# Optimization experiments

Hardware: AMD Instinct MI355X
Metric: run time of the kernel (lower is better)

## Reference

```python
import jax, jax.numpy as jnp
import numpy as np

DIM = 128
D_STATE = 16
EXPAND = 2
E = DIM * EXPAND
BSZ, H, W = 16, 64, 64
LN_EPS = 1e-5


def setup_inputs() -> dict:
    key = jax.random.key(0)
    ks = jax.random.split(key, 8)
    s_in = 1.0 / np.sqrt(DIM)
    s_out = 1.0 / np.sqrt(E)
    return {
        "x": jax.random.normal(ks[0], (BSZ, DIM, H, W), jnp.float32),
        "A": jax.random.normal(ks[1], (D_STATE, D_STATE), jnp.float32) * 0.1,
        "Bm": jax.random.normal(ks[2], (D_STATE, E), jnp.float32) * 0.1,
        "Cm": jax.random.normal(ks[3], (E, D_STATE), jnp.float32) * 0.1,
        "D": jax.random.normal(ks[4], (E,), jnp.float32) * 0.1,
        "W_in": jax.random.uniform(ks[5], (E, DIM), jnp.float32, -s_in, s_in),
        "b_in": jnp.zeros((E,), jnp.float32),
        "W_out": jax.random.uniform(ks[6], (DIM, E), jnp.float32, -s_out, s_out),
        "b_out": jnp.zeros((DIM,), jnp.float32),
        "gamma": jnp.ones((DIM,), jnp.float32),
        "beta": jnp.zeros((DIM,), jnp.float32),
    }


def reference(x, A, Bm, Cm, D, W_in, b_in, W_out, b_out, gamma, beta):
    # x: [B, C, H, W]; dropout is inference-mode identity
    Bsz, C, Hh, Ww = x.shape
    residual = x
    h = x.transpose(0, 2, 3, 1).reshape(Bsz, Hh * Ww, C)  # [B, L, C]
    # LayerNorm over channel dim
    mu = jnp.mean(h, axis=-1, keepdims=True)
    var = jnp.mean((h - mu) ** 2, axis=-1, keepdims=True)
    hn = (h - mu) * jax.lax.rsqrt(var + LN_EPS) * gamma + beta
    # in_proj
    z = jnp.einsum('blc,ec->ble', hn, W_in) + b_in  # [B, L, E]
    # precompute input drive for the recurrence: x_t @ B.T
    u = jnp.einsum('ble,se->bls', z, Bm)  # [B, L, S]
    u_tm = u.transpose(1, 0, 2)  # [L, B, S] time-major for scan

    def step(state, u_t):
        state = jnp.tanh(state @ A.T + u_t)
        return state, state

    init = jnp.zeros((Bsz, A.shape[0]), z.dtype)
    _, states = jax.lax.scan(step, init, u_tm)  # states: [L, B, S]
    states = states.transpose(1, 0, 2)  # [B, L, S]
    y = jnp.einsum('bls,es->ble', states, Cm) + z * D  # [B, L, E]
    out = jnp.einsum('ble,ce->blc', y, W_out) + b_out  # [B, L, C]
    out = out.reshape(Bsz, Hh, Ww, C).transpose(0, 3, 1, 2)
    return out + residual
```

## Files before the change

kernel.cpp:

```cpp
#include <hip/hip_runtime.h>
#include <cstdint>

#define BATCH 16
#define CDIM  128
#define EDIM  256
#define SDIM  16
#define LSEQ  4096
#define LN_EPS 1e-5f

typedef __attribute__((ext_vector_type(8))) short short8;
typedef __attribute__((ext_vector_type(4))) float f32x4;
typedef __attribute__((ext_vector_type(4))) unsigned int u32x4;

#define BIASC  20480
#define BU     20608
#define WCF    20736
#define WUF    41216
#define U_OFF  65536

static __device__ __forceinline__ unsigned short f2bf(float f) {
    uint32_t u = __float_as_uint(f);
    uint32_t r = u + 0x7fffu + ((u >> 16) & 1u);
    return (unsigned short)(r >> 16);
}
static __device__ __forceinline__ float bf2f(unsigned short h) {
    return __uint_as_float(((uint32_t)h) << 16);
}
static __device__ __forceinline__ uint32_t pack_split_trunc(float v) {
    uint32_t u = __float_as_uint(v);
    float hi_f = __uint_as_float(u & 0xffff0000u);
    unsigned short lo = f2bf(v - hi_f);
    return (u >> 16) | ((uint32_t)lo << 16);
}

union U4S8 { u32x4 u; short8 s; };

static __device__ __forceinline__ uint32_t permb(uint32_t a, uint32_t b, uint32_t sel) {
    return __builtin_amdgcn_perm(a, b, sel);
}

static __device__ __forceinline__ void load_bfrag(const uint32_t* row, int cb, int sw,
                                                  short8& bh, short8& bl) {
    u32x4 A = *reinterpret_cast<const u32x4*>(&row[(cb) ^ sw]);
    u32x4 B = *reinterpret_cast<const u32x4*>(&row[(cb + 4) ^ sw]);
    U4S8 h, l;
    h.u[0] = permb(A[1], A[0], 0x05040100u);
    h.u[1] = permb(A[3], A[2], 0x05040100u);
    h.u[2] = permb(B[1], B[0], 0x05040100u);
    h.u[3] = permb(B[3], B[2], 0x05040100u);
    l.u[0] = permb(A[1], A[0], 0x07060302u);
    l.u[1] = permb(A[3], A[2], 0x07060302u);
    l.u[2] = permb(B[1], B[0], 0x07060302u);
    l.u[3] = permb(B[3], B[2], 0x07060302u);
    bh = h.s; bl = l.s;
}

#define MFMA(acc, a, b) acc = __builtin_amdgcn_mfma_f32_16x16x32_bf16((a), (b), (acc), 0, 0, 0)

#define ROT_I(VAL, K) __builtin_amdgcn_mov_dpp((VAL), 0x120 + (K), 0xF, 0xF, true)
#define REP15(M) M(1) M(2) M(3) M(4) M(5) M(6) M(7) M(8) M(9) M(10) M(11) M(12) M(13) M(14) M(15)

#if __has_builtin(__builtin_amdgcn_rcpf)
  #define RCPF(x) __builtin_amdgcn_rcpf(x)
#else
  #define RCPF(x) (1.0f / (x))
#endif

#define SCAN_STEP(ST, UT) { \
    float a0 = fmaf(Ak[0], (ST), (UT)); \
    float a1 = 0.f, a2 = 0.f, a3 = 0.f; \
    { \
        float r_; \
        r_ = __int_as_float(ROT_I(__float_as_int(ST), 1));  a1 = fmaf(Ak[1],  r_, a1); \
        r_ = __int_as_float(ROT_I(__float_as_int(ST), 2));  a2 = fmaf(Ak[2],  r_, a2); \
        r_ = __int_as_float(ROT_I(__float_as_int(ST), 3));  a3 = fmaf(Ak[3],  r_, a3); \
        r_ = __int_as_float(ROT_I(__float_as_int(ST), 4));  a0 = fmaf(Ak[4],  r_, a0); \
        r_ = __int_as_float(ROT_I(__float_as_int(ST), 5));  a1 = fmaf(Ak[5],  r_, a1); \
        r_ = __int_as_float(ROT_I(__float_as_int(ST), 6));  a2 = fmaf(Ak[6],  r_, a2); \
        r_ = __int_as_float(ROT_I(__float_as_int(ST), 7));  a3 = fmaf(Ak[7],  r_, a3); \
        r_ = __int_as_float(ROT_I(__float_as_int(ST), 8));  a0 = fmaf(Ak[8],  r_, a0); \
        r_ = __int_as_float(ROT_I(__float_as_int(ST), 9));  a1 = fmaf(Ak[9],  r_, a1); \
        r_ = __int_as_float(ROT_I(__float_as_int(ST), 10)); a2 = fmaf(Ak[10], r_, a2); \
        r_ = __int_as_float(ROT_I(__float_as_int(ST), 11)); a3 = fmaf(Ak[11], r_, a3); \
        r_ = __int_as_float(ROT_I(__float_as_int(ST), 12)); a0 = fmaf(Ak[12], r_, a0); \
        r_ = __int_as_float(ROT_I(__float_as_int(ST), 13)); a1 = fmaf(Ak[13], r_, a1); \
        r_ = __int_as_float(ROT_I(__float_as_int(ST), 14)); a2 = fmaf(Ak[14], r_, a2); \
        r_ = __int_as_float(ROT_I(__float_as_int(ST), 15)); a3 = fmaf(Ak[15], r_, a3); \
    } \
    float X = (a0 + a2) + (a1 + a3); \
    float ex = __expf(X + X); \
    (ST) = fmaf(-2.f, RCPF(ex + 1.f), 1.f); }

__global__ __launch_bounds__(256) void prep_kernel(
    const float* __restrict__ Bm, const float* __restrict__ Cm,
    const float* __restrict__ Dv, const float* __restrict__ W_in,
    const float* __restrict__ b_in, const float* __restrict__ W_out,
    const float* __restrict__ b_out, float* __restrict__ ws)
{
    uint32_t* wsu = (uint32_t*)ws;
    int blk = blockIdx.x, tid = threadIdx.x;
    if (blk < 40) {
        int widx = blk * 256 + tid;
        int j2 = widx & 3;
        int l  = (widx >> 2) & 63;
        int mf = (widx >> 8) & 7;
        int kt = widx >> 11;
        int row = mf * 16 + (l & 15);
        int k0 = kt * 32 + ((l >> 4) << 3) + j2 * 2;
        float v0 = 0.f, v1 = 0.f;
        if (kt < 4) {
            #pragma unroll 4
            for (int e = 0; e < EDIM; ++e) {
                float wd = W_out[row * EDIM + e] * Dv[e];
                v0 = fmaf(wd, W_in[e * CDIM + k0], v0);
                v1 = fmaf(wd, W_in[e * CDIM + k0 + 1], v1);
            }
        } else {
            int s0 = k0 - 128;
            if (s0 < 16) {
                #pragma unroll 4
                for (int e = 0; e < EDIM; ++e) {
                    float wo = W_out[row * EDIM + e];
                    v0 = fmaf(wo, Cm[e * SDIM + s0], v0);
                    v1 = fmaf(wo, Cm[e * SDIM + s0 + 1], v1);
                }
            }
        }
        unsigned short h0 = f2bf(v0), h1 = f2bf(v1);
        unsigned short l0 = f2bf(v0 - bf2f(h0));
        unsigned short l1 = f2bf(v1 - bf2f(h1));
        wsu[WCF + widx]         = (uint32_t)h0 | ((uint32_t)h1 << 16);
        wsu[WCF + 10240 + widx] = (uint32_t)l0 | ((uint32_t)l1 << 16);
    } else if (blk < 44) {
        int widx = (blk - 40) * 256 + tid;
        int j2 = widx & 3;
        int l  = (widx >> 2) & 63;
        int kt = (widx >> 8) & 3;
        int row = l & 15;
        int k0 = kt * 32 + ((l >> 4) << 3) + j2 * 2;
        float v0 = 0.f, v1 = 0.f;
        #pragma unroll 4
        for (int e = 0; e < EDIM; ++e) {
            float bm = Bm[row * EDIM + e];
            v0 = fmaf(bm, W_in[e * CDIM + k0], v0);
            v1 = fmaf(bm, W_in[e * CDIM + k0 + 1], v1);
        }
        unsigned short h0 = f2bf(v0), h1 = f2bf(v1);
        unsigned short l0 = f2bf(v0 - bf2f(h0));
        unsigned short l1 = f2bf(v1 - bf2f(h1));
        wsu[WUF + widx]        = (uint32_t)h0 | ((uint32_t)h1 << 16);
        wsu[WUF + 1024 + widx] = (uint32_t)l0 | ((uint32_t)l1 << 16);
    } else {
        if (tid < 128) {
            float acc = b_out[tid];
            #pragma unroll 4
            for (int e = 0; e < EDIM; ++e)
                acc += W_out[tid * EDIM + e] * Dv[e] * b_in[e];
            ws[BIASC + tid] = acc;
        } else if (tid < 144) {
            int s = tid - 128;
            float acc = 0.f;
            #pragma unroll 4
            for (int e = 0; e < EDIM; ++e)
                acc += Bm[s * EDIM + e] * b_in[e];
            ws[BU + s] = acc;
        }
    }
}

__global__ __launch_bounds__(256) void halo_kernel(
    const float* __restrict__ x, const float* __restrict__ gamma,
    const float* __restrict__ beta, float* __restrict__ ws)
{
    __shared__ uint32_t xs2[32 * 128];
    __shared__ float pr1[4][32], pr2[4][32];
    __shared__ float mu2[32], rs2[32];
    __shared__ float ulh[32 * 16];

    int t = threadIdx.x;
    int lane = t & 63, wv = t >> 6;
    int blk = blockIdx.x;
    int b  = blk >> 5;
    int P0 = (blk & 31) << 7;
    const float* xb = x + ((size_t)b * CDIM) * LSEQ + P0 + 96;
    const uint32_t* wsu = (const uint32_t*)ws;

    int q4 = 4 * ((t >> 3) & 7);
    f32x4 xr[4];
    float sm0=0.f,sm1=0.f,sm2=0.f,sm3=0.f, sq0=0.f,sq1=0.f,sq2=0.f,sq3=0.f;
    #pragma unroll
    for (int it = 0; it < 4; ++it) {
        int c = (t & 7) + 32 * wv + 8 * it;
        f32x4 v = *reinterpret_cast<const f32x4*>(xb + (size_t)c * LSEQ + q4);
        xr[it] = v;
        sm0 += v[0]; sq0 += v[0]*v[0];
        sm1 += v[1]; sq1 += v[1]*v[1];
        sm2 += v[2]; sq2 += v[2]*v[2];
        sm3 += v[3]; sq3 += v[3]*v[3];
    }
    sm0 += __shfl_xor(sm0,1); sm0 += __shfl_xor(sm0,2); sm0 += __shfl_xor(sm0,4);
    sm1 += __shfl_xor(sm1,1); sm1 += __shfl_xor(sm1,2); sm1 += __shfl_xor(sm1,4);
    sm2 += __shfl_xor(sm2,1); sm2 += __shfl_xor(sm2,2); sm2 += __shfl_xor(sm2,4);
    sm3 += __shfl_xor(sm3,1); sm3 += __shfl_xor(sm3,2); sm3 += __shfl_xor(sm3,4);
    sq0 += __shfl_xor(sq0,1); sq0 += __shfl_xor(sq0,2); sq0 += __shfl_xor(sq0,4);
    sq1 += __shfl_xor(sq1,1); sq1 += __shfl_xor(sq1,2); sq1 += __shfl_xor(sq1,4);
    sq2 += __shfl_xor(sq2,1); sq2 += __shfl_xor(sq2,2); sq2 += __shfl_xor(sq2,4);
    sq3 += __shfl_xor(sq3,1); sq3 += __shfl_xor(sq3,2); sq3 += __shfl_xor(sq3,4);
    if ((lane & 7) == 0) {
        pr1[wv][q4+0] = sm0; pr2[wv][q4+0] = sq0;
        pr1[wv][q4+1] = sm1; pr2[wv][q4+1] = sq1;
        pr1[wv][q4+2] = sm2; pr2[wv][q4+2] = sq2;
        pr1[wv][q4+3] = sm3; pr2[wv][q4+3] = sq3;
    }
    __syncthreads();
    if (t < 32) {
        float s1 = pr1[0][t] + pr1[1][t] + pr1[2][t] + pr1[3][t];
        float s2 = pr2[0][t] + pr2[1][t] + pr2[2][t] + pr2[3][t];
        float mu = s1 * (1.f / 128.f);
        float var = s2 * (1.f / 128.f) - mu * mu;
        mu2[t] = mu; rs2[t] = rsqrtf(var + LN_EPS);
    }
    __syncthreads();

    {
        float mu_[4], rs_[4];
        #pragma unroll
        for (int j = 0; j < 4; ++j) { mu_[j] = mu2[q4+j]; rs_[j] = rs2[q4+j]; }
        #pragma unroll
        for (int it = 0; it < 4; ++it) {
            int c = (t & 7) + 32 * wv + 8 * it;
            float g = gamma[c], be = beta[c];
            #pragma unroll
            for (int j = 0; j < 4; ++j) {
                int q = q4 + j;
                float val = (xr[it][j] - mu_[j]) * rs_[j] * g + be;
                xs2[q * 128 + (c ^ (((q >> 1) & 7) << 2))] = pack_split_trunc(val);
            }
        }
    }
    __syncthreads();

    if (wv < 2) {
        short8 auh[4], aul[4];
        #pragma unroll
        for (int kt = 0; kt < 4; ++kt) {
            U4S8 tt;
            tt.u = *reinterpret_cast<const u32x4*>(&wsu[WUF + kt * 256 + lane * 4]);
            auh[kt] = tt.s;
            tt.u = *reinterpret_cast<const u32x4*>(&wsu[WUF + 1024 + kt * 256 + lane * 4]);
            aul[kt] = tt.s;
        }
        int q = wv * 16 + (lane & 15);
        const uint32_t* row = xs2 + q * 128;
        int sw = ((q >> 1) & 7) << 2;
        f32x4 acc = {0.f, 0.f, 0.f, 0.f};
        #pragma unroll
        for (int kt = 0; kt < 4; ++kt) {
            short8 bh, bl;
            load_bfrag(row, kt * 32 + ((lane >> 4) << 3), sw, bh, bl);
            MFMA(acc, auh[kt], bh);
            MFMA(acc, auh[kt], bl);
            MFMA(acc, aul[kt], bh);
        }
        int s4 = (lane >> 4) << 2;
        f32x4 bu4 = *reinterpret_cast<const f32x4*>(ws + BU + s4);
        #pragma unroll
        for (int j = 0; j < 4; ++j)
            ulh[q * 16 + s4 + j] = acc[j] + bu4[j];
    }
    __syncthreads();
    if (t < 128)
        *reinterpret_cast<f32x4*>(ws + U_OFF + (size_t)blk * 512 + t * 4) =
            *reinterpret_cast<const f32x4*>(ulh + t * 4);
}

__global__ __launch_bounds__(256, 2) void fused_kernel(
    const float* __restrict__ x, const float* __restrict__ Amat,
    const float* __restrict__ gamma, const float* __restrict__ beta,
    float* __restrict__ out, const float* __restrict__ ws)
{
    __shared__ uint32_t xs[16384];
    __shared__ unsigned short ul[160 * 18];
    __shared__ unsigned short stl[128 * 32];
    __shared__ float mu_s[128], sig_s[128];

    int t = threadIdx.x;
    int lane = t & 63, wv = t >> 6;
    int blk = blockIdx.x;
    int b  = blk >> 5;
    int P0 = (blk & 31) << 7;
    const float* xb = x   + ((size_t)b * CDIM) * LSEQ + P0;
    float*       ob = out + ((size_t)b * CDIM) * LSEQ + P0;
    const uint32_t* wsu = (const uint32_t*)ws;

    int p4 = 4 * (t >> 3);
    {
        f32x4 xr[16];
        float sm0=0.f,sm1=0.f,sm2=0.f,sm3=0.f, sq0=0.f,sq1=0.f,sq2=0.f,sq3=0.f;
        #pragma unroll
        for (int it = 0; it < 16; ++it) {
            int c = (t & 7) + 8 * it;
            f32x4 v = *reinterpret_cast<const f32x4*>(xb + (size_t)c * LSEQ + p4);
            xr[it] = v;
            sm0 += v[0]; sq0 += v[0]*v[0];
            sm1 += v[1]; sq1 += v[1]*v[1];
            sm2 += v[2]; sq2 += v[2]*v[2];
            sm3 += v[3]; sq3 += v[3]*v[3];
        }
        sm0 += __shfl_xor(sm0,1); sm0 += __shfl_xor(sm0,2); sm0 += __shfl_xor(sm0,4);
        sm1 += __shfl_xor(sm1,1); sm1 += __shfl_xor(sm1,2); sm1 += __shfl_xor(sm1,4);
        sm2 += __shfl_xor(sm2,1); sm2 += __shfl_xor(sm2,2); sm2 += __shfl_xor(sm2,4);
        sm3 += __shfl_xor(sm3,1); sm3 += __shfl_xor(sm3,2); sm3 += __shfl_xor(sm3,4);
        sq0 += __shfl_xor(sq0,1); sq0 += __shfl_xor(sq0,2); sq0 += __shfl_xor(sq0,4);
        sq1 += __shfl_xor(sq1,1); sq1 += __shfl_xor(sq1,2); sq1 += __shfl_xor(sq1,4);
        sq2 += __shfl_xor(sq2,1); sq2 += __shfl_xor(sq2,2); sq2 += __shfl_xor(sq2,4);
        sq3 += __shfl_xor(sq3,1); sq3 += __shfl_xor(sq3,2); sq3 += __shfl_xor(sq3,4);
        float mu_[4], rs_[4], sg_[4];
        {
            float smv[4] = {sm0, sm1, sm2, sm3};
            float sqv[4] = {sq0, sq1, sq2, sq3};
            #pragma unroll
            for (int j = 0; j < 4; ++j) {
                float mu = smv[j] * (1.f / 128.f);
                float var = sqv[j] * (1.f / 128.f) - mu * mu;
                float rs = rsqrtf(var + LN_EPS);
                mu_[j] = mu; rs_[j] = rs; sg_[j] = RCPF(rs);
            }
        }
        if ((lane & 7) == 0) {
            #pragma unroll
            for (int j = 0; j < 4; ++j) { mu_s[p4+j] = mu_[j]; sig_s[p4+j] = sg_[j]; }
        }
        #pragma unroll
        for (int it = 0; it < 16; ++it) {
            int c = (t & 7) + 8 * it;
            float g = gamma[c], be = beta[c];
            #pragma unroll
            for (int j = 0; j < 4; ++j) {
                int p = p4 + j;
                float val = (xr[it][j] - mu_[j]) * rs_[j] * g + be;
                xs[p * 128 + (c ^ (((p >> 1) & 7) << 2))] = pack_split_trunc(val);
            }
        }
    }
    __syncthreads();

    {
        if (t < 128) {
            int src = (blk & 31) ? (blk - 1) : (blk > 0 ? blk : 0);
            f32x4 v = *reinterpret_cast<const f32x4*>(ws + U_OFF + (size_t)src * 512 + t * 4);
            int q = t >> 2, s0 = (t & 3) * 4;
            #pragma unroll
            for (int k = 0; k < 4; ++k)
                ul[q * 18 + s0 + k] = f2bf(v[k]);
        }
        {
            uint32_t* stl32 = (uint32_t*)stl;
            int p = t >> 1, k0 = 8 + (t & 1) * 4;
            u32x4 z = {0u,0u,0u,0u};
            *reinterpret_cast<u32x4*>(&stl32[p * 16 + k0]) = z;
        }
        short8 auh[4], aul[4];
        #pragma unroll
        for (int kt = 0; kt < 4; ++kt) {
            U4S8 tt;
            tt.u = *reinterpret_cast<const u32x4*>(&wsu[WUF + kt * 256 + lane * 4]);
            auh[kt] = tt.s;
            tt.u = *reinterpret_cast<const u32x4*>(&wsu[WUF + 1024 + kt * 256 + lane * 4]);
            aul[kt] = tt.s;
        }
        int s4 = (lane >> 4) << 2;
        f32x4 bu4 = *reinterpret_cast<const f32x4*>(ws + BU + s4);
        #pragma unroll
        for (int nfi = 0; nfi < 2; ++nfi) {
            int nf = wv * 2 + nfi;
            int p = nf * 16 + (lane & 15);
            const uint32_t* row = xs + p * 128;
            int sw = ((p >> 1) & 7) << 2;
            f32x4 acc = {0.f, 0.f, 0.f, 0.f};
            #pragma unroll
            for (int kt = 0; kt < 4; ++kt) {
                short8 bh, bl;
                load_bfrag(row, kt * 32 + ((lane >> 4) << 3), sw, bh, bl);
                MFMA(acc, auh[kt], bh);
                MFMA(acc, auh[kt], bl);
                MFMA(acc, aul[kt], bh);
            }
            #pragma unroll
            for (int j = 0; j < 4; ++j)
                ul[(32 + p) * 18 + s4 + j] = f2bf(acc[j] + bu4[j]);
        }
    }
    __syncthreads();

    {
        int s = t & 15, g = t >> 4;
        float Ak[16];
        Ak[0] = Amat[s * 16 + s];
        {
            int pk;
            #define PERMLOAD(K) pk = ROT_I(s, K); Ak[K] = Amat[s * 16 + pk];
            REP15(PERMLOAD)
            #undef PERMLOAD
        }
        int r0 = 8 * g;
        float ub[8];
        #pragma unroll
        for (int j = 0; j < 8; ++j) ub[j] = bf2f(ul[(r0 + j) * 18 + s]);
        int rl = r0 + 8;
        int tbase = P0 + 8 * g - 32;
        float st = 0.f;
        #pragma unroll
        for (int it = 0; it < 4; ++it) {
            #pragma unroll
            for (int j = 0; j < 8; ++j) {
                float u_t = (tbase + it * 8 + j >= 0) ? ub[j] : 0.f;
                ub[j] = bf2f(ul[rl * 18 + s]);
                ++rl;
                SCAN_STEP(st, u_t)
            }
        }
        #pragma unroll
        for (int j = 0; j < 8; ++j) {
            SCAN_STEP(st, ub[j])
            stl[(r0 + j) * 32 + s] = f2bf(st);
        }
    }
    __syncthreads();

    int wm = wv >> 1, wn = wv & 1;
    f32x4 acc[4][4];
    #pragma unroll
    for (int mf = 0; mf < 4; ++mf)
        #pragma unroll
        for (int nfl = 0; nfl < 4; ++nfl) { f32x4 z = {0.f,0.f,0.f,0.f}; acc[mf][nfl] = z; }

    #pragma unroll 2
    for (int kt = 0; kt < 4; ++kt) {
        short8 ah[4], al[4];
        #pragma unroll
        for (int mf = 0; mf < 4; ++mf) {
            int mfg = wm * 4 + mf;
            U4S8 tt;
            tt.u = *reinterpret_cast<const u32x4*>(&wsu[WCF + (kt * 8 + mfg) * 256 + lane * 4]);
            ah[mf] = tt.s;
            tt.u = *reinterpret_cast<const u32x4*>(&wsu[WCF + 10240 + (kt * 8 + mfg) * 256 + lane * 4]);
            al[mf] = tt.s;
        }
        #pragma unroll
        for (int nfl = 0; nfl < 4; ++nfl) {
            int p = (wn * 4 + nfl) * 16 + (lane & 15);
            const uint32_t* row = xs + p * 128;
            short8 bh, bl;
            load_bfrag(row, kt * 32 + ((lane >> 4) << 3), ((p >> 1) & 7) << 2, bh, bl);
            #pragma unroll
            for (int mf = 0; mf < 4; ++mf) {
                MFMA(acc[mf][nfl], ah[mf], bh);
                MFMA(acc[mf][nfl], ah[mf], bl);
                MFMA(acc[mf][nfl], al[mf], bh);
            }
        }
    }
    {
        short8 ah[4];
        #pragma unroll
        for (int mf = 0; mf < 4; ++mf) {
            int mfg = wm * 4 + mf;
            U4S8 tt;
            tt.u = *reinterpret_cast<const u32x4*>(&wsu[WCF + (32 + mfg) * 256 + lane * 4]);
            ah[mf] = tt.s;
        }
        int grp = lane >> 4;
        #pragma unroll
        for (int nfl = 0; nfl < 4; ++nfl) {
            int p = (wn * 4 + nfl) * 16 + (lane & 15);
            U4S8 tt;
            tt.u = *reinterpret_cast<const u32x4*>(&stl[p * 32 + grp * 8]);
            short8 bs = tt.s;
            #pragma unroll
            for (int mf = 0; mf < 4; ++mf)
                MFMA(acc[mf][nfl], ah[mf], bs);
        }
    }

    {
        int q4 = (lane >> 4) << 2;
        float sgp[4], mup[4];
        #pragma unroll
        for (int nfl = 0; nfl < 4; ++nfl) {
            int p = (wn * 4 + nfl) * 16 + (lane & 15);
            sgp[nfl] = sig_s[p]; mup[nfl] = mu_s[p];
        }
        #pragma unroll
        for (int mf = 0; mf < 4; ++mf) {
            int cb = wm * 64 + mf * 16 + q4;
            f32x4 bc = *reinterpret_cast<const f32x4*>(ws + BIASC + cb);
            #pragma unroll
            for (int j = 0; j < 4; ++j) {
                int c = cb + j;
                float ig = RCPF(gamma[c]);
                float be = beta[c];
                size_t rowa = (size_t)c * LSEQ;
                #pragma unroll
                for (int nfl = 0; nfl < 4; ++nfl) {
                    int p = (wn * 4 + nfl) * 16 + (lane & 15);
                    uint32_t w = xs[p * 128 + (c ^ (((p >> 1) & 7) << 2))];
                    float hn = __uint_as_float(w << 16) + __uint_as_float(w & 0xffff0000u);
                    float xrc = fmaf((hn - be) * ig, sgp[nfl], mup[nfl]);
                    float val = acc[mf][nfl][j] + bc[j] + xrc;
                    __builtin_nontemporal_store(val, &ob[rowa + p]);
                }
            }
        }
    }
}

extern "C" void kernel_launch(void* const* d_in, const int* in_sizes, int n_in,
                              void* d_out, int out_size, void* d_ws, size_t ws_size,
                              hipStream_t stream)
{
    const float* x     = (const float*)d_in[0];
    const float* A     = (const float*)d_in[1];
    const float* Bm    = (const float*)d_in[2];
    const float* Cm    = (const float*)d_in[3];
    const float* Dv    = (const float*)d_in[4];
    const float* W_in  = (const float*)d_in[5];
    const float* b_in  = (const float*)d_in[6];
    const float* W_out = (const float*)d_in[7];
    const float* b_out = (const float*)d_in[8];
    const float* gamma = (const float*)d_in[9];
    const float* beta  = (const float*)d_in[10];
    float* ws  = (float*)d_ws;
    float* out = (float*)d_out;

    prep_kernel <<<dim3(45),  dim3(256), 0, stream>>>(Bm, Cm, Dv, W_in, b_in, W_out, b_out, ws);
    halo_kernel <<<dim3(512), dim3(256), 0, stream>>>(x, gamma, beta, ws);
    fused_kernel<<<dim3(512), dim3(256), 0, stream>>>(x, A, gamma, beta, out, ws);
}
```

Measured before the change: 139.6 us.

## Drop split-bf16 GEMMs, fuse halo into main kernel, re-read residual from global

```diff
diff --git a/kernel.cpp b/kernel.cpp
--- a/kernel.cpp
+++ b/kernel.cpp
@@ -16,7 +16,6 @@
 #define BU     20608
 #define WCF    20736
 #define WUF    41216
-#define U_OFF  65536
 
 static __device__ __forceinline__ unsigned short f2bf(float f) {
     uint32_t u = __float_as_uint(f);
@@ -26,34 +25,11 @@
 static __device__ __forceinline__ float bf2f(unsigned short h) {
     return __uint_as_float(((uint32_t)h) << 16);
 }
-static __device__ __forceinline__ uint32_t pack_split_trunc(float v) {
-    uint32_t u = __float_as_uint(v);
-    float hi_f = __uint_as_float(u & 0xffff0000u);
-    unsigned short lo = f2bf(v - hi_f);
-    return (u >> 16) | ((uint32_t)lo << 16);
+static __device__ __forceinline__ uint32_t pack2bf(float a, float b) {
+    return (uint32_t)f2bf(a) | ((uint32_t)f2bf(b) << 16);
 }
 
 union U4S8 { u32x4 u; short8 s; };
-
-static __device__ __forceinline__ uint32_t permb(uint32_t a, uint32_t b, uint32_t sel) {
-    return __builtin_amdgcn_perm(a, b, sel);
-}
-
-static __device__ __forceinline__ void load_bfrag(const uint32_t* row, int cb, int sw,
-                                                  short8& bh, short8& bl) {
-    u32x4 A = *reinterpret_cast<const u32x4*>(&row[(cb) ^ sw]);
-    u32x4 B = *reinterpret_cast<const u32x4*>(&row[(cb + 4) ^ sw]);
-    U4S8 h, l;
-    h.u[0] = permb(A[1], A[0], 0x05040100u);
-    h.u[1] = permb(A[3], A[2], 0x05040100u);
-    h.u[2] = permb(B[1], B[0], 0x05040100u);
-    h.u[3] = permb(B[3], B[2], 0x05040100u);
-    l.u[0] = permb(A[1], A[0], 0x07060302u);
-    l.u[1] = permb(A[3], A[2], 0x07060302u);
-    l.u[2] = permb(B[1], B[0], 0x07060302u);
-    l.u[3] = permb(B[3], B[2], 0x07060302u);
-    bh = h.s; bl = l.s;
-}
 
 #define MFMA(acc, a, b) acc = __builtin_amdgcn_mfma_f32_16x16x32_bf16((a), (b), (acc), 0, 0, 0)
 
@@ -126,11 +102,7 @@
                 }
             }
         }
-        unsigned short h0 = f2bf(v0), h1 = f2bf(v1);
-        unsigned short l0 = f2bf(v0 - bf2f(h0));
-        unsigned short l1 = f2bf(v1 - bf2f(h1));
-        wsu[WCF + widx]         = (uint32_t)h0 | ((uint32_t)h1 << 16);
-        wsu[WCF + 10240 + widx] = (uint32_t)l0 | ((uint32_t)l1 << 16);
+        wsu[WCF + widx] = pack2bf(v0, v1);
     } else if (blk < 44) {
         int widx = (blk - 40) * 256 + tid;
         int j2 = widx & 3;
@@ -145,11 +117,7 @@
             v0 = fmaf(bm, W_in[e * CDIM + k0], v0);
             v1 = fmaf(bm, W_in[e * CDIM + k0 + 1], v1);
         }
-        unsigned short h0 = f2bf(v0), h1 = f2bf(v1);
-        unsigned short l0 = f2bf(v0 - bf2f(h0));
-        unsigned short l1 = f2bf(v1 - bf2f(h1));
-        wsu[WUF + widx]        = (uint32_t)h0 | ((uint32_t)h1 << 16);
-        wsu[WUF + 1024 + widx] = (uint32_t)l0 | ((uint32_t)l1 << 16);
+        wsu[WUF + widx] = pack2bf(v0, v1);
     } else {
         if (tid < 128) {
             float acc = b_out[tid];
@@ -168,227 +136,112 @@
     }
 }
 
-__global__ __launch_bounds__(256) void halo_kernel(
-    const float* __restrict__ x, const float* __restrict__ gamma,
-    const float* __restrict__ beta, float* __restrict__ ws)
+__global__ __launch_bounds__(256, 2) void fused_kernel(
+    const float* __restrict__ x, const float* __restrict__ Amat,
+    const float* __restrict__ gamma, const float* __restrict__ beta,
+    float* __restrict__ out, const float* __restrict__ ws)
 {
-    __shared__ uint32_t xs2[32 * 128];
-    __shared__ float pr1[4][32], pr2[4][32];
-    __shared__ float mu2[32], rs2[32];
-    __shared__ float ulh[32 * 16];
+    __shared__ unsigned short xs_h[160 * 136];
+    __shared__ unsigned short ul[160 * 18];
+    __shared__ unsigned short stl[128 * 40];
 
     int t = threadIdx.x;
     int lane = t & 63, wv = t >> 6;
     int blk = blockIdx.x;
     int b  = blk >> 5;
     int P0 = (blk & 31) << 7;
-    const float* xb = x + ((size_t)b * CDIM) * LSEQ + P0 + 96;
+    const float* xg = x + ((size_t)b * CDIM) * LSEQ;
+    float*       ob = out + ((size_t)b * CDIM) * LSEQ + P0;
     const uint32_t* wsu = (const uint32_t*)ws;
-
-    int q4 = 4 * ((t >> 3) & 7);
-    f32x4 xr[4];
-    float sm0=0.f,sm1=0.f,sm2=0.f,sm3=0.f, sq0=0.f,sq1=0.f,sq2=0.f,sq3=0.f;
-    #pragma unroll
-    for (int it = 0; it < 4; ++it) {
-        int c = (t & 7) + 32 * wv + 8 * it;
-        f32x4 v = *reinterpret_cast<const f32x4*>(xb + (size_t)c * LSEQ + q4);
-        xr[it] = v;
-        sm0 += v[0]; sq0 += v[0]*v[0];
-        sm1 += v[1]; sq1 += v[1]*v[1];
-        sm2 += v[2]; sq2 += v[2]*v[2];
-        sm3 += v[3]; sq3 += v[3]*v[3];
-    }
-    sm0 += __shfl_xor(sm0,1); sm0 += __shfl_xor(sm0,2); sm0 += __shfl_xor(sm0,4);
-    sm1 += __shfl_xor(sm1,1); sm1 += __shfl_xor(sm1,2); sm1 += __shfl_xor(sm1,4);
-    sm2 += __shfl_xor(sm2,1); sm2 += __shfl_xor(sm2,2); sm2 += __shfl_xor(sm2,4);
-    sm3 += __shfl_xor(sm3,1); sm3 += __shfl_xor(sm3,2); sm3 += __shfl_xor(sm3,4);
-    sq0 += __shfl_xor(sq0,1); sq0 += __shfl_xor(sq0,2); sq0 += __shfl_xor(sq0,4);
-    sq1 += __shfl_xor(sq1,1); sq1 += __shfl_xor(sq1,2); sq1 += __shfl_xor(sq1,4);
-    sq2 += __shfl_xor(sq2,1); sq2 += __shfl_xor(sq2,2); sq2 += __shfl_xor(sq2,4);
-    sq3 += __shfl_xor(sq3,1); sq3 += __shfl_xor(sq3,2); sq3 += __shfl_xor(sq3,4);
-    if ((lane & 7) == 0) {
-        pr1[wv][q4+0] = sm0; pr2[wv][q4+0] = sq0;
-        pr1[wv][q4+1] = sm1; pr2[wv][q4+1] = sq1;
-        pr1[wv][q4+2] = sm2; pr2[wv][q4+2] = sq2;
-        pr1[wv][q4+3] = sm3; pr2[wv][q4+3] = sq3;
+    uint32_t* xs32 = (uint32_t*)xs_h;
+
+    {
+        int cslot = t & 15, pg = t >> 4;
+        int cb = cslot * 8;
+        f32x4 g0 = *reinterpret_cast<const f32x4*>(&gamma[cb]);
+        f32x4 g1 = *reinterpret_cast<const f32x4*>(&gamma[cb + 4]);
+        f32x4 be0 = *reinterpret_cast<const f32x4*>(&beta[cb]);
+        f32x4 be1 = *reinterpret_cast<const f32x4*>(&beta[cb + 4]);
+        #pragma unroll
+        for (int pit = 0; pit < 3; ++pit) {
+            int p4 = 4 * (pg + 16 * pit);
+            if (p4 < 160) {
+                int gp4 = P0 - 32 + p4; if (gp4 < 0) gp4 = 0;
+                f32x4 xr[8];
+                #pragma unroll
+                for (int i = 0; i < 8; ++i)
+                    xr[i] = *reinterpret_cast<const f32x4*>(xg + (size_t)(cb + i) * LSEQ + gp4);
+                float sm[4] = {0.f,0.f,0.f,0.f}, sq[4] = {0.f,0.f,0.f,0.f};
+                #pragma unroll
+                for (int i = 0; i < 8; ++i)
+                    #pragma unroll
+                    for (int j = 0; j < 4; ++j) {
+                        float v = xr[i][j];
+                        sm[j] += v; sq[j] += v * v;
+                    }
+                #pragma unroll
+                for (int j = 0; j < 4; ++j) {
+                    sm[j] += __shfl_xor(sm[j], 1); sq[j] += __shfl_xor(sq[j], 1);
+                    sm[j] += __shfl_xor(sm[j], 2); sq[j] += __shfl_xor(sq[j], 2);
+                    sm[j] += __shfl_xor(sm[j], 4); sq[j] += __shfl_xor(sq[j], 4);
+                    sm[j] += __shfl_xor(sm[j], 8); sq[j] += __shfl_xor(sq[j], 8);
+                }
+                #pragma unroll
+                for (int j = 0; j < 4; ++j) {
+                    float mu = sm[j] * (1.f / 128.f);
+                    float var = sq[j] * (1.f / 128.f) - mu * mu;
+                    float rs = rsqrtf(var + LN_EPS);
+                    u32x4 w;
+                    #pragma unroll
+                    for (int i2 = 0; i2 < 4; ++i2) {
+                        float a0 = (xr[2*i2][j]   - mu) * rs;
+                        float a1 = (xr[2*i2+1][j] - mu) * rs;
+                        float gA = (2*i2   < 4) ? g0[2*i2]       : g1[2*i2-4];
+                        float gB = (2*i2+1 < 4) ? g0[2*i2+1]     : g1[2*i2-3];
+                        float bA = (2*i2   < 4) ? be0[2*i2]      : be1[2*i2-4];
+                        float bB = (2*i2+1 < 4) ? be0[2*i2+1]    : be1[2*i2-3];
+                        w[i2] = pack2bf(fmaf(a0, gA, bA), fmaf(a1, gB, bB));
+                    }
+                    *reinterpret_cast<u32x4*>(&xs32[(p4 + j) * 68 + cslot * 4]) = w;
+                }
+            }
+        }
     }
     __syncthreads();
-    if (t < 32) {
-        float s1 = pr1[0][t] + pr1[1][t] + pr1[2][t] + pr1[3][t];
-        float s2 = pr2[0][t] + pr2[1][t] + pr2[2][t] + pr2[3][t];
-        float mu = s1 * (1.f / 128.f);
-        float var = s2 * (1.f / 128.f) - mu * mu;
-        mu2[t] = mu; rs2[t] = rsqrtf(var + LN_EPS);
-    }
-    __syncthreads();
-
-    {
-        float mu_[4], rs_[4];
-        #pragma unroll
-        for (int j = 0; j < 4; ++j) { mu_[j] = mu2[q4+j]; rs_[j] = rs2[q4+j]; }
-        #pragma unroll
-        for (int it = 0; it < 4; ++it) {
-            int c = (t & 7) + 32 * wv + 8 * it;
-            float g = gamma[c], be = beta[c];
-            #pragma unroll
-            for (int j = 0; j < 4; ++j) {
-                int q = q4 + j;
-                float val = (xr[it][j] - mu_[j]) * rs_[j] * g + be;
-                xs2[q * 128 + (c ^ (((q >> 1) & 7) << 2))] = pack_split_trunc(val);
-            }
-        }
-    }
-    __syncthreads();
-
-    if (wv < 2) {
-        short8 auh[4], aul[4];
+
+    {
+        if (t < 128) {
+            uint32_t* stl32 = (uint32_t*)stl;
+            u32x4 z = {0u,0u,0u,0u};
+            *reinterpret_cast<u32x4*>(&stl32[t * 20 + 8]) = z;
+            *reinterpret_cast<u32x4*>(&stl32[t * 20 + 12]) = z;
+        }
+        short8 au[4];
         #pragma unroll
         for (int kt = 0; kt < 4; ++kt) {
             U4S8 tt;
             tt.u = *reinterpret_cast<const u32x4*>(&wsu[WUF + kt * 256 + lane * 4]);
-            auh[kt] = tt.s;
-            tt.u = *reinterpret_cast<const u32x4*>(&wsu[WUF + 1024 + kt * 256 + lane * 4]);
-            aul[kt] = tt.s;
-        }
-        int q = wv * 16 + (lane & 15);
-        const uint32_t* row = xs2 + q * 128;
-        int sw = ((q >> 1) & 7) << 2;
-        f32x4 acc = {0.f, 0.f, 0.f, 0.f};
-        #pragma unroll
-        for (int kt = 0; kt < 4; ++kt) {
-            short8 bh, bl;
-            load_bfrag(row, kt * 32 + ((lane >> 4) << 3), sw, bh, bl);
-            MFMA(acc, auh[kt], bh);
-            MFMA(acc, auh[kt], bl);
-            MFMA(acc, aul[kt], bh);
+            au[kt] = tt.s;
         }
         int s4 = (lane >> 4) << 2;
         f32x4 bu4 = *reinterpret_cast<const f32x4*>(ws + BU + s4);
         #pragma unroll
-        for (int j = 0; j < 4; ++j)
-            ulh[q * 16 + s4 + j] = acc[j] + bu4[j];
-    }
-    __syncthreads();
-    if (t < 128)
-        *reinterpret_cast<f32x4*>(ws + U_OFF + (size_t)blk * 512 + t * 4) =
-            *reinterpret_cast<const f32x4*>(ulh + t * 4);
-}
-
-__global__ __launch_bounds__(256, 2) void fused_kernel(
-    const float* __restrict__ x, const float* __restrict__ Amat,
-    const float* __restrict__ gamma, const float* __restrict__ beta,
-    float* __restrict__ out, const float* __restrict__ ws)
-{
-    __shared__ uint32_t xs[16384];
-    __shared__ unsigned short ul[160 * 18];
-    __shared__ unsigned short stl[128 * 32];
-    __shared__ float mu_s[128], sig_s[128];
-
-    int t = threadIdx.x;
-    int lane = t & 63, wv = t >> 6;
-    int blk = blockIdx.x;
-    int b  = blk >> 5;
-    int P0 = (blk & 31) << 7;
-    const float* xb = x   + ((size_t)b * CDIM) * LSEQ + P0;
-    float*       ob = out + ((size_t)b * CDIM) * LSEQ + P0;
-    const uint32_t* wsu = (const uint32_t*)ws;
-
-    int p4 = 4 * (t >> 3);
-    {
-        f32x4 xr[16];
-        float sm0=0.f,sm1=0.f,sm2=0.f,sm3=0.f, sq0=0.f,sq1=0.f,sq2=0.f,sq3=0.f;
-        #pragma unroll
-        for (int it = 0; it < 16; ++it) {
-            int c = (t & 7) + 8 * it;
-            f32x4 v = *reinterpret_cast<const f32x4*>(xb + (size_t)c * LSEQ + p4);
-            xr[it] = v;
-            sm0 += v[0]; sq0 += v[0]*v[0];
-            sm1 += v[1]; sq1 += v[1]*v[1];
-            sm2 += v[2]; sq2 += v[2]*v[2];
-            sm3 += v[3]; sq3 += v[3]*v[3];
-        }
-        sm0 += __shfl_xor(sm0,1); sm0 += __shfl_xor(sm0,2); sm0 += __shfl_xor(sm0,4);
-        sm1 += __shfl_xor(sm1,1); sm1 += __shfl_xor(sm1,2); sm1 += __shfl_xor(sm1,4);
-        sm2 += __shfl_xor(sm2,1); sm2 += __shfl_xor(sm2,2); sm2 += __shfl_xor(sm2,4);
-        sm3 += __shfl_xor(sm3,1); sm3 += __shfl_xor(sm3,2); sm3 += __shfl_xor(sm3,4);
-        sq0 += __shfl_xor(sq0,1); sq0 += __shfl_xor(sq0,2); sq0 += __shfl_xor(sq0,4);
-        sq1 += __shfl_xor(sq1,1); sq1 += __shfl_xor(sq1,2); sq1 += __shfl_xor(sq1,4);
-        sq2 += __shfl_xor(sq2,1); sq2 += __shfl_xor(sq2,2); sq2 += __shfl_xor(sq2,4);
-        sq3 += __shfl_xor(sq3,1); sq3 += __shfl_xor(sq3,2); sq3 += __shfl_xor(sq3,4);
-        float mu_[4], rs_[4], sg_[4];
-        {
-            float smv[4] = {sm0, sm1, sm2, sm3};
-            float sqv[4] = {sq0, sq1, sq2, sq3};
-            #pragma unroll
-            for (int j = 0; j < 4; ++j) {
-                float mu = smv[j] * (1.f / 128.f);
-                float var = sqv[j] * (1.f / 128.f) - mu * mu;
-                float rs = rsqrtf(var + LN_EPS);
-                mu_[j] = mu; rs_[j] = rs; sg_[j] = RCPF(rs);
-            }
-        }
-        if ((lane & 7) == 0) {
-            #pragma unroll
-            for (int j = 0; j < 4; ++j) { mu_s[p4+j] = mu_[j]; sig_s[p4+j] = sg_[j]; }
-        }
-        #pragma unroll
-        for (int it = 0; it < 16; ++it) {
-            int c = (t & 7) + 8 * it;
-            float g = gamma[c], be = beta[c];
-            #pragma unroll
-            for (int j = 0; j < 4; ++j) {
-                int p = p4 + j;
-                float val = (xr[it][j] - mu_[j]) * rs_[j] * g + be;
-                xs[p * 128 + (c ^ (((p >> 1) & 7) << 2))] = pack_split_trunc(val);
-            }
-        }
-    }
-    __syncthreads();
-
-    {
-        if (t < 128) {
-            int src = (blk & 31) ? (blk - 1) : (blk > 0 ? blk : 0);
-            f32x4 v = *reinterpret_cast<const f32x4*>(ws + U_OFF + (size_t)src * 512 + t * 4);
-            int q = t >> 2, s0 = (t & 3) * 4;
-            #pragma unroll
-            for (int k = 0; k < 4; ++k)
-                ul[q * 18 + s0 + k] = f2bf(v[k]);
-        }
-        {
-            uint32_t* stl32 = (uint32_t*)stl;
-            int p = t >> 1, k0 = 8 + (t & 1) * 4;
-            u32x4 z = {0u,0u,0u,0u};
-            *reinterpret_cast<u32x4*>(&stl32[p * 16 + k0]) = z;
-        }
-        short8 auh[4], aul[4];
-        #pragma unroll
-        for (int kt = 0; kt < 4; ++kt) {
-            U4S8 tt;
-            tt.u = *reinterpret_cast<const u32x4*>(&wsu[WUF + kt * 256 + lane * 4]);
-            auh[kt] = tt.s;
-            tt.u = *reinterpret_cast<const u32x4*>(&wsu[WUF + 1024 + kt * 256 + lane * 4]);
-            aul[kt] = tt.s;
-        }
-        int s4 = (lane >> 4) << 2;
-        f32x4 bu4 = *reinterpret_cast<const f32x4*>(ws + BU + s4);
-        #pragma unroll
-        for (int nfi = 0; nfi < 2; ++nfi) {
-            int nf = wv * 2 + nfi;
-            int p = nf * 16 + (lane & 15);
-            const uint32_t* row = xs + p * 128;
-            int sw = ((p >> 1) & 7) << 2;
-            f32x4 acc = {0.f, 0.f, 0.f, 0.f};
-            #pragma unroll
-            for (int kt = 0; kt < 4; ++kt) {
-                short8 bh, bl;
-                load_bfrag(row, kt * 32 + ((lane >> 4) << 3), sw, bh, bl);
-                MFMA(acc, auh[kt], bh);
-                MFMA(acc, auh[kt], bl);
-                MFMA(acc, aul[kt], bh);
-            }
-            #pragma unroll
-            for (int j = 0; j < 4; ++j)
-                ul[(32 + p) * 18 + s4 + j] = f2bf(acc[j] + bu4[j]);
+        for (int i = 0; i < 3; ++i) {
+            int nf = wv + 4 * i;
+            if (nf < 10) {
+                int r = nf * 16 + (lane & 15);
+                const uint32_t* row = xs32 + r * 68;
+                f32x4 acc = {0.f, 0.f, 0.f, 0.f};
+                #pragma unroll
+                for (int kt = 0; kt < 4; ++kt) {
+                    U4S8 tt;
+                    tt.u = *reinterpret_cast<const u32x4*>(&row[kt * 16 + ((lane >> 4) << 2)]);
+                    MFMA(acc, au[kt], tt.s);
+                }
+                #pragma unroll
+                for (int j = 0; j < 4; ++j)
+                    ul[r * 18 + s4 + j] = f2bf(acc[j] + bu4[j]);
+            }
         }
     }
     __syncthreads();
@@ -408,7 +261,7 @@
         #pragma unroll
         for (int j = 0; j < 8; ++j) ub[j] = bf2f(ul[(r0 + j) * 18 + s]);
         int rl = r0 + 8;
-        int tbase = P0 + 8 * g - 32;
+        int tbase = P0 - 32 + r0;
         float st = 0.f;
         #pragma unroll
         for (int it = 0; it < 4; ++it) {
@@ -423,91 +276,72 @@
         #pragma unroll
         for (int j = 0; j < 8; ++j) {
             SCAN_STEP(st, ub[j])
-            stl[(r0 + j) * 32 + s] = f2bf(st);
+            stl[(r0 + j) * 40 + s] = f2bf(st);
         }
     }
     __syncthreads();
 
     int wm = wv >> 1, wn = wv & 1;
+    int grp = lane >> 4;
     f32x4 acc[4][4];
     #pragma unroll
     for (int mf = 0; mf < 4; ++mf)
         #pragma unroll
         for (int nfl = 0; nfl < 4; ++nfl) { f32x4 z = {0.f,0.f,0.f,0.f}; acc[mf][nfl] = z; }
 
-    #pragma unroll 2
+    #pragma unroll
     for (int kt = 0; kt < 4; ++kt) {
-        short8 ah[4], al[4];
+        short8 ah[4];
         #pragma unroll
         for (int mf = 0; mf < 4; ++mf) {
-            int mfg = wm * 4 + mf;
-            U4S8 tt;
-            tt.u = *reinterpret_cast<const u32x4*>(&wsu[WCF + (kt * 8 + mfg) * 256 + lane * 4]);
+            U4S8 tt;
+            tt.u = *reinterpret_cast<const u32x4*>(&wsu[WCF + (kt * 8 + wm * 4 + mf) * 256 + lane * 4]);
             ah[mf] = tt.s;
-            tt.u = *reinterpret_cast<const u32x4*>(&wsu[WCF + 10240 + (kt * 8 + mfg) * 256 + lane * 4]);
-            al[mf] = tt.s;
         }
         #pragma unroll
         for (int nfl = 0; nfl < 4; ++nfl) {
             int p = (wn * 4 + nfl) * 16 + (lane & 15);
-            const uint32_t* row = xs + p * 128;
-            short8 bh, bl;
-            load_bfrag(row, kt * 32 + ((lane >> 4) << 3), ((p >> 1) & 7) << 2, bh, bl);
+            U4S8 tt;
+            tt.u = *reinterpret_cast<const u32x4*>(&xs32[(32 + p) * 68 + kt * 16 + grp * 4]);
             #pragma unroll
-            for (int mf = 0; mf < 4; ++mf) {
-                MFMA(acc[mf][nfl], ah[mf], bh);
-                MFMA(acc[mf][nfl], ah[mf], bl);
-                MFMA(acc[mf][nfl], al[mf], bh);
-            }
-        }
-    }
-    {
+            for (int mf = 0; mf < 4; ++mf)
+                MFMA(acc[mf][nfl], ah[mf], tt.s);
+        }
+    }
+    {
+        const uint32_t* stl32 = (const uint32_t*)stl;
         short8 ah[4];
         #pragma unroll
         for (int mf = 0; mf < 4; ++mf) {
-            int mfg = wm * 4 + mf;
-            U4S8 tt;
-            tt.u = *reinterpret_cast<const u32x4*>(&wsu[WCF + (32 + mfg) * 256 + lane * 4]);
+            U4S8 tt;
+            tt.u = *reinterpret_cast<const u32x4*>(&wsu[WCF + (32 + wm * 4 + mf) * 256 + lane * 4]);
             ah[mf] = tt.s;
         }
-        int grp = lane >> 4;
         #pragma unroll
         for (int nfl = 0; nfl < 4; ++nfl) {
             int p = (wn * 4 + nfl) * 16 + (lane & 15);
             U4S8 tt;
-            tt.u = *reinterpret_cast<const u32x4*>(&stl[p * 32 + grp * 8]);
-            short8 bs = tt.s;
+            tt.u = *reinterpret_cast<const u32x4*>(&stl32[p * 20 + grp * 4]);
             #pragma unroll
             for (int mf = 0; mf < 4; ++mf)
-                MFMA(acc[mf][nfl], ah[mf], bs);
-        }
-    }
-
-    {
-        int q4 = (lane >> 4) << 2;
-        float sgp[4], mup[4];
-        #pragma unroll
-        for (int nfl = 0; nfl < 4; ++nfl) {
-            int p = (wn * 4 + nfl) * 16 + (lane & 15);
-            sgp[nfl] = sig_s[p]; mup[nfl] = mu_s[p];
-        }
+                MFMA(acc[mf][nfl], ah[mf], tt.s);
+        }
+    }
+
+    {
+        const float* xb2 = xg + P0;
+        int q4 = grp << 2;
         #pragma unroll
         for (int mf = 0; mf < 4; ++mf) {
-            int cb = wm * 64 + mf * 16 + q4;
-            f32x4 bc = *reinterpret_cast<const f32x4*>(ws + BIASC + cb);
+            int cb2 = wm * 64 + mf * 16 + q4;
+            f32x4 bc = *reinterpret_cast<const f32x4*>(ws + BIASC + cb2);
             #pragma unroll
             for (int j = 0; j < 4; ++j) {
-                int c = cb + j;
-                float ig = RCPF(gamma[c]);
-                float be = beta[c];
-                size_t rowa = (size_t)c * LSEQ;
+                size_t rowa = (size_t)(cb2 + j) * LSEQ;
                 #pragma unroll
                 for (int nfl = 0; nfl < 4; ++nfl) {
                     int p = (wn * 4 + nfl) * 16 + (lane & 15);
-                    uint32_t w = xs[p * 128 + (c ^ (((p >> 1) & 7) << 2))];
-                    float hn = __uint_as_float(w << 16) + __uint_as_float(w & 0xffff0000u);
-                    float xrc = fmaf((hn - be) * ig, sgp[nfl], mup[nfl]);
-                    float val = acc[mf][nfl][j] + bc[j] + xrc;
+                    float val = acc[mf][nfl][j] + bc[j] + xb2[rowa + p];
                     __builtin_nontemporal_store(val, &ob[rowa + p]);
                 }
             }
@@ -534,6 +368,5 @@
     float* out = (float*)d_out;
 
     prep_kernel <<<dim3(45),  dim3(256), 0, stream>>>(Bm, Cm, Dv, W_in, b_in, W_out, b_out, ws);
-    halo_kernel <<<dim3(512), dim3(256), 0, stream>>>(x, gamma, beta, ws);
     fused_kernel<<<dim3(512), dim3(256), 0, stream>>>(x, A, gamma, beta, out, ws);
 }
```

Measured after the change: 134.4 us. 1.04x faster.
